# Performance work log

Measured on AMD Instinct MI355X. Metric: run time of the kernel, lower is better.

The kernel has to match this reference:

```python
import jax, jax.numpy as jnp
import numpy as np

S = 32
D = S * S          # d = 1024 grid points
DK = 64
R = 4              # heads
NB = 3             # blocks
IN_DIM = 64
EPS = 1e-5
DX = 2.0 / (S - 1)
DXDY = DX * DX
SCALE = 1.0 / np.sqrt(float(DK))


def _edge():
    # grid[i,j] = (gx[i], gx[j]); gridT is the transpose ordering
    gx = jnp.linspace(-1.0, 1.0, S, dtype=jnp.float32)
    g = jnp.stack(jnp.meshgrid(gx, gx, indexing='ij'), axis=-1)  # [S,S,2]
    grid = g.reshape(D, 2)
    gridT = g.transpose(1, 0, 2).reshape(D, 2)
    return jnp.concatenate([
        jnp.broadcast_to(grid[:, None, :], (D, D, 2)),
        jnp.broadcast_to(gridT[None, :, :], (D, D, 2)),
    ], axis=-1)  # [D, D, 4]


def _mlp(e, W1, b1, W2, b2, W3, b3):
    # DenseNet([4,32,64,1], LeakyReLU): two hidden LeakyReLU layers, linear head
    h = jax.nn.leaky_relu(e @ W1 + b1)
    h = jax.nn.leaky_relu(h @ W2 + b2)
    return h @ W3 + b3


def _ln(v, g, b):
    # LayerNorm over normalized_shape [2d, input_dim] -> reduce last two axes
    m = jnp.mean(v, axis=(1, 2), keepdims=True)
    var = jnp.var(v, axis=(1, 2), keepdims=True)
    return (v - m) * jax.lax.rsqrt(var + EPS) * g + b


def setup_inputs() -> dict:
    key = jax.random.key(0)
    ks = jax.random.split(key, 24)
    f32 = jnp.float32

    def nrm(k, shape, fan):
        return jax.random.normal(k, shape, f32) / np.sqrt(float(fan))

    inp = {
        'x': jax.random.normal(ks[0], (8, D, 1), f32),
        'xy': jax.random.normal(ks[1], (8, 2 * D, IN_DIM), f32),
        'P': jnp.zeros((1,), f32),
        # kernel MLP (edge -> weight)
        'kW1': nrm(ks[2], (4, 32), 4), 'kb1': jnp.zeros((32,), f32),
        'kW2': nrm(ks[3], (32, 64), 32), 'kb2': jnp.zeros((64,), f32),
        'kW3': nrm(ks[4], (64, 1), 64), 'kb3': jnp.zeros((1,), f32),
        # kernelf MLP (edge -> weightf)
        'fW1': nrm(ks[5], (4, 32), 4), 'fb1': jnp.zeros((32,), f32),
        'fW2': nrm(ks[6], (32, 64), 32), 'fb2': jnp.zeros((64,), f32),
        'fW3': nrm(ks[7], (64, 1), 64), 'fb3': jnp.zeros((1,), f32),
        # per-(block, head) Q/K linear layers
        'Wq': nrm(ks[8], (NB, R, IN_DIM, DK), IN_DIM),
        'bq': jnp.zeros((NB, R, DK), f32),
        'Wk': nrm(ks[9], (NB, R, IN_DIM, DK), IN_DIM),
        'bk': jnp.zeros((NB, R, DK), f32),
        # per-block LayerNorm affine params over [2d, input_dim]
        'ln_g': jnp.ones((NB, 2 * D, IN_DIM), f32),
        'ln_b': jnp.zeros((NB, 2 * D, IN_DIM), f32),
    }
    return inp


def _forward(x, xy, P, kW1, kb1, kW2, kb2, kW3, kb3,
             fW1, fb1, fW2, fb2, fW3, fb3, Wq, bq, Wk, bk, ln_g, ln_b):
    edge = _edge()
    weight = _mlp(edge, kW1, kb1, kW2, kb2, kW3, kb3).reshape(D, D)   # shared over batch
    weightf = _mlp(edge, fW1, fb1, fW2, fb2, fW3, fb3).reshape(D, D)

    Vinput = _ln(xy, ln_g[0], ln_b[0])  # [b, 2d, in]

    for j in range(NB - 1):
        mid = jnp.zeros_like(Vinput)
        for i in range(R):
            Q = Vinput @ Wq[j, i] + bq[j, i]  # [b, 2d, dk]
            K = Vinput @ Wk[j, i] + bk[j, i]
            Attn = jnp.einsum('bnk,bmk->bnm', Q, K) * SCALE  # [b, 2d, 2d]
            mid = mid + DXDY * jnp.einsum('bnm,bmi->bni', Attn, Vinput)
        Vinput = _ln(mid, ln_g[j + 1], ln_b[j + 1]) + Vinput

    b = xy.shape[0]
    out = jnp.zeros((b, IN_DIM, D), xy.dtype)
    xy_d = xy[:, :D, :]  # [b, d, in]
    for i in range(R):
        Q = Vinput @ Wq[NB - 1, i] + bq[NB - 1, i]
        K = Vinput @ Wk[NB - 1, i] + bk[NB - 1, i]
        Au = jnp.einsum('bnk,bmk->bnm', Q[:, :D], K[:, :D]) * SCALE  # Attn[:, :d, :d]
        Af = jnp.einsum('bnk,bmk->bnm', Q[:, D:], K[:, :D]) * SCALE  # Attn[:, d:, :d]
        Vu = DXDY * jnp.einsum('bnm,bmi->bin', Au, xy_d)  # [b, in, d]
        Vf = DXDY * jnp.einsum('bnm,bmi->bin', Af, xy_d)
        out = out + DXDY * (Vu @ weight) + DXDY * (Vf @ weightf)
    return out.transpose(0, 2, 1)  # [b, d, in]


def reference(x, xy, P, kW1, kb1, kW2, kb2, kW3, kb3,
              fW1, fb1, fW2, fb2, fW3, fb3, Wq, bq, Wk, bk, ln_g, ln_b):
    return _forward(x, xy, P, kW1, kb1, kW2, kb2, kW3, kb3,
                    fW1, fb1, fW2, fb2, fW3, fb3, Wq, bq, Wk, bk, ln_g, ln_b)
```

## Files before the change

kernel.cpp:

```cpp
#include <hip/hip_runtime.h>

namespace {
constexpr int SD = 1024;
constexpr int TD = 2048;
constexpr int BATCH = 8;
constexpr int RH = 4;
constexpr float EPSc = 1e-5f;
constexpr float DXf = 2.0f / 31.0f;
constexpr float DXDYf = DXf * DXf;
constexpr float SCALEf = 0.125f;
constexpr float CFINAL = DXDYf * DXDYf * SCALEf;

constexpr size_t OFF_V   = 0;
constexpr size_t OFF_MID = OFF_V   + (size_t)BATCH * TD * 64;
constexpr size_t OFF_W   = OFF_MID + (size_t)BATCH * TD * 64;
constexpr size_t OFF_WF  = OFF_W   + (size_t)SD * SD;
constexpr size_t OFF_U1K = OFF_WF  + (size_t)SD * SD;
constexpr size_t OFF_U2K = OFF_U1K + SD * 32;
constexpr size_t OFF_U1F = OFF_U2K + SD * 32;
constexpr size_t OFF_U2F = OFF_U1F + SD * 32;
constexpr size_t OFF_GP  = OFF_U2F + SD * 32;
constexpr size_t OFF_SP  = OFF_GP  + (size_t)BATCH * 32 * 4096;
constexpr size_t OFF_A   = OFF_SP  + BATCH * 32 * 64;
constexpr size_t OFF_RV  = OFF_A   + BATCH * 4096;
constexpr size_t OFF_LNP = OFF_RV  + BATCH * 64;
constexpr size_t OFF_ZU  = OFF_LNP + BATCH * 32 * 2;
constexpr size_t OFF_ZF  = OFF_ZU  + (size_t)SD * 512;
constexpr size_t OFF_W1  = OFF_ZF  + (size_t)SD * 512;
constexpr size_t OFF_CS  = OFF_W1  + SD;
constexpr size_t WS_FLOATS = OFF_CS + 16 * SD;
constexpr size_t LIN_OFF = 50704;
}

typedef __bf16 bf16x8 __attribute__((ext_vector_type(8)));
typedef float f32x4 __attribute__((ext_vector_type(4)));

__device__ __forceinline__ float leaky(float x) { return fmaxf(x, 0.01f * x); }
__device__ __forceinline__ float gxv(int i) { return -1.0f + (2.0f / 31.0f) * (float)i; }
__device__ __forceinline__ ushort f2bf(float x) { union { __bf16 b; ushort u; } v; v.b = (__bf16)x; return v.u; }
__device__ __forceinline__ float bf2f(ushort u) { return __uint_as_float(((uint)u) << 16); }

__global__ __launch_bounds__(256) void k_prep(
    const float* __restrict__ kW1, const float* __restrict__ kb1,
    const float* __restrict__ fW1, const float* __restrict__ fb1,
    float* __restrict__ u1k, float* __restrict__ u2k,
    float* __restrict__ u1f, float* __restrict__ u2f,
    const float* __restrict__ kW2, const float* __restrict__ kW3, const float* __restrict__ kb2,
    const float* __restrict__ fW2, const float* __restrict__ fW3, const float* __restrict__ fb2,
    float* __restrict__ LIN,
    const float* __restrict__ Wq, const float* __restrict__ bq,
    const float* __restrict__ Wk, const float* __restrict__ bk,
    float* __restrict__ Ep, float* __restrict__ fp,
    float* __restrict__ gp, float* __restrict__ cp,
    const float* __restrict__ xy, float* __restrict__ part) {
  __shared__ __align__(16) float Wqs[4096];
  __shared__ float Wks[64 * 65];
  __shared__ float bqs[64], bks[64];
  __shared__ float ss4[4], qq4[4];
  int blk = blockIdx.x, t = threadIdx.x;
  if (blk >= 16) {
    int idx = blk - 16;
    int b = idx >> 5, c = idx & 31;
    const float4* X4 = reinterpret_cast<const float4*>(xy + (size_t)b * 131072 + (size_t)c * 4096);
    float s = 0.f, q = 0.f;
#pragma unroll
    for (int k = 0; k < 4; k++) {
      float4 v = X4[t + k * 256];
      s += v.x + v.y + v.z + v.w;
      q += v.x * v.x + v.y * v.y + v.z * v.z + v.w * v.w;
    }
    for (int off = 32; off; off >>= 1) { s += __shfl_down(s, off); q += __shfl_down(q, off); }
    int lane = t & 63, wid = t >> 6;
    if (lane == 0) { ss4[wid] = s; qq4[wid] = q; }
    __syncthreads();
    if (t == 0) {
      part[(size_t)(b * 32 + c) * 2] = ss4[0] + ss4[1] + ss4[2] + ss4[3];
      part[(size_t)(b * 32 + c) * 2 + 1] = qq4[0] + qq4[1] + qq4[2] + qq4[3];
    }
    return;
  }
  if (blk < 4) {
    int n = blk * 256 + t;
    float ga = gxv(n >> 5), gb = gxv(n & 31);
    for (int j = 0; j < 32; j++) {
      u1k[n * 32 + j] = ga * kW1[j] + gb * kW1[32 + j] + kb1[j];
      u2k[n * 32 + j] = gb * kW1[64 + j] + ga * kW1[96 + j];
      u1f[n * 32 + j] = ga * fW1[j] + gb * fW1[32 + j] + fb1[j];
      u2f[n * 32 + j] = gb * fW1[64 + j] + ga * fW1[96 + j];
    }
    if (blk < 2 && t < 33) {
      const float* W2 = blk ? fW2 : kW2;
      const float* W3 = blk ? fW3 : kW3;
      const float* b2 = blk ? fb2 : kb2;
      if (t < 32) {
        float s = 0.f;
        for (int o = 0; o < 64; o++) s += W2[t * 64 + o] * W3[o];
        LIN[blk * 32 + t] = s;
      } else {
        float s = 0.f;
        for (int o = 0; o < 64; o++) s += b2[o] * W3[o];
        LIN[64 + blk] = s;
      }
    }
    return;
  }
  int h = blk - 4;
  const float* wqb = Wq + (size_t)h * 4096;
  const float* wkb = Wk + (size_t)h * 4096;
  for (int idx = t; idx < 4096; idx += 256) {
    Wqs[idx] = wqb[idx];
    Wks[(idx >> 6) * 65 + (idx & 63)] = wkb[idx];
  }
  if (t < 64) { bqs[t] = bq[h * 64 + t]; bks[t] = bk[h * 64 + t]; }
  __syncthreads();
  int cpp = t & 63, cb = (t >> 6) * 16;
  float acc[16];
#pragma unroll
  for (int u = 0; u < 16; u++) acc[u] = 0.f;
  for (int k = 0; k < 64; k++) {
    float wkv = Wks[cpp * 65 + k];
#pragma unroll
    for (int u = 0; u < 16; u++) acc[u] += Wqs[(cb + u) * 64 + k] * wkv;
  }
  float* eo = Ep + (size_t)h * 4096;
#pragma unroll
  for (int u = 0; u < 16; u++) eo[(cb + u) * 64 + cpp] = acc[u];
  if (t < 64) {
    float f = 0.f, gg = 0.f;
    for (int k = 0; k < 64; k++) {
      f  += Wqs[t * 64 + k] * bks[k];
      gg += Wks[t * 65 + k] * bqs[k];
    }
    fp[h * 64 + t] = f;
    gp[h * 64 + t] = gg;
    float ca = bqs[t] * bks[t];
    ca += __shfl_xor(ca, 1, 64);
    ca += __shfl_xor(ca, 2, 64);
    ca += __shfl_xor(ca, 4, 64);
    ca += __shfl_xor(ca, 8, 64);
    ca += __shfl_xor(ca, 16, 64);
    ca += __shfl_xor(ca, 32, 64);
    if (t == 0) cp[h] = ca;
  }
}

__global__ __launch_bounds__(256) void k_mlp2(
    const float* __restrict__ u1k, const float* __restrict__ u2k,
    const float* __restrict__ kW2, const float* __restrict__ kb2,
    const float* __restrict__ kW3, const float* __restrict__ kb3,
    const float* __restrict__ u1f, const float* __restrict__ u2f,
    const float* __restrict__ fW2, const float* __restrict__ fb2,
    const float* __restrict__ fW3, const float* __restrict__ fb3,
    const float* __restrict__ LIN,
    ushort* __restrict__ outK, ushort* __restrict__ outF) {
  const int which = blockIdx.y;
  const float* u1 = which ? u1f : u1k;
  const float* u2 = which ? u2f : u2k;
  const float* W2 = which ? fW2 : kW2;
  const float* b2 = which ? fb2 : kb2;
  const float* W3 = which ? fW3 : kW3;
  const float* b3 = which ? fb3 : kb3;
  ushort* out = which ? outF : outK;

  const int t = threadIdx.x;
  const int lane = t & 63, wave = t >> 6;
  const int row = lane & 15, grp = lane >> 4;
  const int n0 = (blockIdx.x >> 1) * 2;
  const int mh = blockIdx.x & 1;

  bf16x8 wfrag[4];
  float4 b2q[4], w3q[4];
#pragma unroll
  for (int tt = 0; tt < 4; tt++) {
#pragma unroll
    for (int i = 0; i < 8; i++) wfrag[tt][i] = (__bf16)W2[(grp * 8 + i) * 64 + tt * 16 + row];
    b2q[tt] = *reinterpret_cast<const float4*>(b2 + tt * 16 + grp * 4);
    w3q[tt] = *reinterpret_cast<const float4*>(W3 + tt * 16 + grp * 4);
  }
  float4 l0 = *reinterpret_cast<const float4*>(LIN + which * 32 + grp * 8);
  float4 l1 = *reinterpret_cast<const float4*>(LIN + which * 32 + grp * 8 + 4);
  float linp[8] = {l0.x, l0.y, l0.z, l0.w, l1.x, l1.y, l1.z, l1.w};
  const float cst = 0.505f * LIN[64 + which] + b3[0];

  float u1j[2][8];
#pragma unroll
  for (int nn = 0; nn < 2; nn++)
#pragma unroll
    for (int i = 0; i < 8; i++) u1j[nn][i] = u1[(n0 + nn) * 32 + grp * 8 + i];

#pragma unroll
  for (int chunk = 0; chunk < 2; chunk++) {
#pragma unroll
    for (int st = 0; st < 4; st++) {
      int mbase = mh * 512 + chunk * 256 + wave * 64 + st * 16;
      int m = mbase + row;
      const float4* u2p = reinterpret_cast<const float4*>(u2 + (size_t)m * 32 + grp * 8);
      float4 ua = u2p[0], ub = u2p[1];
      float hv[8] = {ua.x, ua.y, ua.z, ua.w, ub.x, ub.y, ub.z, ub.w};
#pragma unroll
      for (int nn = 0; nn < 2; nn++) {
        float h1f[8];
#pragma unroll
        for (int i = 0; i < 8; i++) h1f[i] = leaky(u1j[nn][i] + hv[i]);
        float accLin = 0.f;
#pragma unroll
        for (int i = 0; i < 8; i++) accLin = fmaf(linp[i], h1f[i], accLin);
        bf16x8 pfrag;
#pragma unroll
        for (int i = 0; i < 8; i++) pfrag[i] = (__bf16)h1f[i];
        float accAbs = 0.f;
#pragma unroll
        for (int tt = 0; tt < 4; tt++) {
          f32x4 ci = {b2q[tt].x, b2q[tt].y, b2q[tt].z, b2q[tt].w};
          f32x4 c = __builtin_amdgcn_mfma_f32_16x16x32_bf16(wfrag[tt], pfrag, ci, 0, 0, 0);
          accAbs = fmaf(fabsf(c[0]), w3q[tt].x, accAbs);
          accAbs = fmaf(fabsf(c[1]), w3q[tt].y, accAbs);
          accAbs = fmaf(fabsf(c[2]), w3q[tt].z, accAbs);
          accAbs = fmaf(fabsf(c[3]), w3q[tt].w, accAbs);
        }
        float red = fmaf(0.495f, accAbs, 0.505f * accLin);
        red += __shfl_xor(red, 16, 64);
        red += __shfl_xor(red, 32, 64);
        if (grp == 0) out[(size_t)(n0 + nn) * SD + mbase + row] = f2bf(red + cst);
      }
    }
  }
}

__global__ __launch_bounds__(256) void k_cvtapply(
    const ushort* __restrict__ srcA, const ushort* __restrict__ srcB,
    ushort* __restrict__ dstA, ushort* __restrict__ dstB,
    const float* __restrict__ src, const float* __restrict__ g,
    const float* __restrict__ bb, const float* __restrict__ lnp,
    float* __restrict__ Vout, float* __restrict__ Gp, float* __restrict__ sp) {
  __shared__ float T[64][65];
  __shared__ __align__(16) float Vs[4096];
  __shared__ float sm[2];
  int blk = blockIdx.x, t = threadIdx.x;
  if (blk < 512) {
    int bx = blk & 15, by = (blk >> 4) & 15, bz = blk >> 8;
    const ushort* srcp = bz ? srcB : srcA;
    ushort* dst = bz ? dstB : dstA;
    int c0 = bx * 64, r0 = by * 64;
    int rr = t >> 2, cc = (t & 3) * 16;
    const uint4* s4 = reinterpret_cast<const uint4*>(srcp + (size_t)(r0 + rr) * 1024 + c0 + cc);
    uint4 q0 = s4[0], q1 = s4[1];
    uint qs[8] = {q0.x, q0.y, q0.z, q0.w, q1.x, q1.y, q1.z, q1.w};
#pragma unroll
    for (int j = 0; j < 8; j++) {
      T[rr][cc + 2 * j]     = bf2f((ushort)(qs[j] & 0xffffu));
      T[rr][cc + 2 * j + 1] = bf2f((ushort)(qs[j] >> 16));
    }
    __syncthreads();
    uint pk[8];
#pragma unroll
    for (int j = 0; j < 8; j++) {
      uint lo = (uint)f2bf(T[cc + 2 * j][rr]);
      uint hi = (uint)f2bf(T[cc + 2 * j + 1][rr]);
      pk[j] = lo | (hi << 16);
    }
    ushort* dp = dst + (size_t)(c0 + rr) * 1024 + r0 + cc;
    uint4* dp4 = reinterpret_cast<uint4*>(dp);
    dp4[0] = make_uint4(pk[0], pk[1], pk[2], pk[3]);
    dp4[1] = make_uint4(pk[4], pk[5], pk[6], pk[7]);
    return;
  }
  int idx2 = blk - 512;
  int c = idx2 & 31, b = idx2 >> 5;
  if (t == 0) {
    float s = 0.f, q = 0.f;
    for (int cc = 0; cc < 32; cc++) {
      s += lnp[(size_t)(b * 32 + cc) * 2];
      q += lnp[(size_t)(b * 32 + cc) * 2 + 1];
    }
    float mean = s / 131072.0f;
    sm[0] = mean;
    sm[1] = rsqrtf(q / 131072.0f - mean * mean + EPSc);
  }
  __syncthreads();
  float mean = sm[0], is = sm[1];
  size_t base4 = (size_t)b * 32768 + (size_t)c * 1024;
#pragma unroll
  for (int k = 0; k < 4; k++) {
    int idx = t + k * 256;
    float4 v = reinterpret_cast<const float4*>(src)[base4 + idx];
    float4 gg = reinterpret_cast<const float4*>(g)[c * 1024 + idx];
    float4 bv = reinterpret_cast<const float4*>(bb)[c * 1024 + idx];
    float4 r;
    r.x = (v.x - mean) * is * gg.x + bv.x;
    r.y = (v.y - mean) * is * gg.y + bv.y;
    r.z = (v.z - mean) * is * gg.z + bv.z;
    r.w = (v.w - mean) * is * gg.w + bv.w;
    reinterpret_cast<float4*>(Vout)[base4 + idx] = r;
    reinterpret_cast<float4*>(Vs)[idx] = r;
  }
  __syncthreads();
  int tp = t >> 4, tq = t & 15;
  float a2[4][4] = {};
  for (int k = 0; k < 64; k++) {
    float4 xv = *reinterpret_cast<const float4*>(&Vs[k * 64 + tp * 4]);
    float4 yv = *reinterpret_cast<const float4*>(&Vs[k * 64 + tq * 4]);
    a2[0][0] += xv.x * yv.x; a2[0][1] += xv.x * yv.y; a2[0][2] += xv.x * yv.z; a2[0][3] += xv.x * yv.w;
    a2[1][0] += xv.y * yv.x; a2[1][1] += xv.y * yv.y; a2[1][2] += xv.y * yv.z; a2[1][3] += xv.y * yv.w;
    a2[2][0] += xv.z * yv.x; a2[2][1] += xv.z * yv.y; a2[2][2] += xv.z * yv.z; a2[2][3] += xv.z * yv.w;
    a2[3][0] += xv.w * yv.x; a2[3][1] += xv.w * yv.y; a2[3][2] += xv.w * yv.z; a2[3][3] += xv.w * yv.w;
  }
  float* go = Gp + (size_t)(b * 32 + c) * 4096;
#pragma unroll
  for (int i = 0; i < 4; i++) {
    float4 w = {a2[i][0], a2[i][1], a2[i][2], a2[i][3]};
    *reinterpret_cast<float4*>(&go[(tp * 4 + i) * 64 + tq * 4]) = w;
  }
  if (t < 64) {
    float s = 0.f;
    for (int k = 0; k < 64; k++) s += Vs[k * 64 + t];
    sp[(size_t)(b * 32 + c) * 64 + t] = s;
  }
}

__global__ __launch_bounds__(256) void k_gred(const float* __restrict__ Gp, const float* __restrict__ sp,
                                              float* __restrict__ G, float* __restrict__ sv, int nch) {
  int blk = blockIdx.x, b = blockIdx.y, t = threadIdx.x;
  int idx = blk * 256 + t;
  float a = 0.f;
  for (int c = 0; c < nch; c++) a += Gp[(size_t)(b * nch + c) * 4096 + idx];
  G[(size_t)b * 4096 + idx] = a;
  if (blk == 0 && t < 64) {
    float s = 0.f;
    for (int c = 0; c < nch; c++) s += sp[(size_t)(b * nch + c) * 64 + t];
    sv[b * 64 + t] = s;
  }
}

__global__ __launch_bounds__(256) void k_headsA2(
    const float* __restrict__ G, const float* __restrict__ sv,
    const float* __restrict__ Ep, const float* __restrict__ fp,
    const float* __restrict__ gp, const float* __restrict__ cp,
    int j, float scale, int doStats,
    float* __restrict__ A, float* __restrict__ RVo, float* __restrict__ STAT) {
  int b = blockIdx.x, t = threadIdx.x;
  __shared__ float Es[64 * 65];
  __shared__ __align__(16) float Gs[4096];
  __shared__ __align__(16) float As[4096];
  __shared__ float ss[64], fs[64], gs[64];
  __shared__ float cj;
  __shared__ float redbuf[8];
  const float* e0 = Ep + (size_t)(j * RH) * 4096;
  for (int idx = t; idx < 4096; idx += 256) {
    float e = e0[idx] + e0[idx + 4096] + e0[idx + 8192] + e0[idx + 12288];
    Es[(idx >> 6) * 65 + (idx & 63)] = e;
    Gs[idx] = G[(size_t)b * 4096 + idx];
  }
  if (t < 64) {
    ss[t] = sv[b * 64 + t];
    int h0 = j * RH * 64;
    fs[t] = fp[h0 + t] + fp[h0 + 64 + t] + fp[h0 + 128 + t] + fp[h0 + 192 + t];
    gs[t] = gp[h0 + t] + gp[h0 + 64 + t] + gp[h0 + 128 + t] + gp[h0 + 192 + t];
  }
  if (t == 0) cj = cp[j * RH] + cp[j * RH + 1] + cp[j * RH + 2] + cp[j * RH + 3];
  __syncthreads();
  int c = t >> 2, qb = (t & 3) * 16;
  float fv = fs[c];
  float4 acc[4];
#pragma unroll
  for (int u = 0; u < 4; u++) {
    acc[u].x = fv * ss[qb + u * 4 + 0];
    acc[u].y = fv * ss[qb + u * 4 + 1];
    acc[u].z = fv * ss[qb + u * 4 + 2];
    acc[u].w = fv * ss[qb + u * 4 + 3];
  }
  for (int d = 0; d < 64; d++) {
    float ev = Es[c * 65 + d];
    const float4* gr = reinterpret_cast<const float4*>(&Gs[d * 64 + qb]);
#pragma unroll
    for (int u = 0; u < 4; u++) {
      float4 gv = gr[u];
      acc[u].x += ev * gv.x; acc[u].y += ev * gv.y; acc[u].z += ev * gv.z; acc[u].w += ev * gv.w;
    }
  }
  float* ao = A + (size_t)b * 4096 + c * 64 + qb;
#pragma unroll
  for (int u = 0; u < 4; u++) {
    float4 v = acc[u];
    v.x *= scale; v.y *= scale; v.z *= scale; v.w *= scale;
    reinterpret_cast<float4*>(ao)[u] = v;
    *reinterpret_cast<float4*>(&As[c * 64 + qb + u * 4]) = v;
  }
  float rv_t = 0.f;
  if (t < 64) {
    float r = cj * ss[t];
    for (int d = 0; d < 64; d++) r += gs[d] * Gs[d * 64 + t];
    r *= scale;
    RVo[b * 64 + t] = r;
    rv_t = r;
  }
  if (!doStats) return;
  __syncthreads();
  float4 h[4] = {};
  for (int d = 0; d < 64; d++) {
    float gvv = Gs[c * 64 + d];
    const float4* ar = reinterpret_cast<const float4*>(&As[d * 64 + qb]);
#pragma unroll
    for (int u = 0; u < 4; u++) {
      float4 av = ar[u];
      h[u].x += gvv * av.x; h[u].y += gvv * av.y; h[u].z += gvv * av.z; h[u].w += gvv * av.w;
    }
  }
  float tp_ = 0.f;
#pragma unroll
  for (int u = 0; u < 4; u++) {
    float4 a = *reinterpret_cast<const float4*>(&As[c * 64 + qb + u * 4]);
    tp_ += a.x * h[u].x + a.y * h[u].y + a.z * h[u].z + a.w * h[u].w;
  }
  tp_ += __shfl_xor(tp_, 1, 64);  tp_ += __shfl_xor(tp_, 2, 64);
  tp_ += __shfl_xor(tp_, 4, 64);  tp_ += __shfl_xor(tp_, 8, 64);
  tp_ += __shfl_xor(tp_, 16, 64); tp_ += __shfl_xor(tp_, 32, 64);
  if ((t & 63) == 0) redbuf[t >> 6] = tp_;
  if (t < 64) {
    float t1 = 0.f;
    for (int d = 0; d < 64; d++) t1 += ss[d] * As[d * 64 + t];
    float s1 = t1, sr = rv_t, sr2 = rv_t * rv_t, srt = rv_t * t1;
#pragma unroll
    for (int off = 1; off < 64; off <<= 1) {
      s1  += __shfl_xor(s1, off, 64);
      sr  += __shfl_xor(sr, off, 64);
      sr2 += __shfl_xor(sr2, off, 64);
      srt += __shfl_xor(srt, off, 64);
    }
    if (t == 0) { redbuf[4] = s1; redbuf[5] = sr; redbuf[6] = sr2; redbuf[7] = srt; }
  }
  __syncthreads();
  if (t == 0) {
    float tr = redbuf[0] + redbuf[1] + redbuf[2] + redbuf[3];
    float smid = redbuf[4] + 2048.0f * redbuf[5];
    float mu = smid / 131072.0f;
    float e2 = (tr + 2.0f * redbuf[7] + 2048.0f * redbuf[6]) / 131072.0f;
    STAT[b * 2] = mu;
    STAT[b * 2 + 1] = rsqrtf(e2 - mu * mu + EPSc);
  }
}

__global__ __launch_bounds__(256) void k_midapply(
    float* __restrict__ V, const float* __restrict__ A,
    const float* __restrict__ RVv, const float* __restrict__ STAT,
    const float* __restrict__ g, const float* __restrict__ bb,
    const float* __restrict__ Yext,
    float* __restrict__ Gp, float* __restrict__ sp, int nchG) {
  int blk = blockIdx.x, b = blockIdx.y, t = threadIdx.x;
  __shared__ __align__(16) float As[4096];
  __shared__ __align__(16) float Vs[4096];
  __shared__ __align__(16) float Ys[4096];
  __shared__ float rs[64];
  __shared__ float sm[2];
  const float4* A4 = reinterpret_cast<const float4*>(A + (size_t)b * 4096);
#pragma unroll
  for (int k = 0; k < 4; k++) reinterpret_cast<float4*>(As)[t + k * 256] = A4[t + k * 256];
  if (t < 64) rs[t] = RVv[b * 64 + t];
  if (t == 0) { sm[0] = STAT[b * 2]; sm[1] = STAT[b * 2 + 1]; }
  bool doG = (blk < nchG);
  if (Yext != nullptr && doG) {
    size_t yb = (size_t)b * 32768 + (size_t)blk * 1024;
#pragma unroll
    for (int k = 0; k < 4; k++)
      reinterpret_cast<float4*>(Ys)[t + k * 256] = reinterpret_cast<const float4*>(Yext)[yb + t + k * 256];
  }
  __syncthreads();
  float mu = sm[0], is = sm[1];
  int rl = t >> 2, qb = (t & 3) * 16;
  int row = blk * 64 + rl;
  float* vr = V + (size_t)b * 131072 + (size_t)row * 64;
  float4 acc[4];
#pragma unroll
  for (int u = 0; u < 4; u++) {
    acc[u].x = rs[qb + u * 4 + 0]; acc[u].y = rs[qb + u * 4 + 1];
    acc[u].z = rs[qb + u * 4 + 2]; acc[u].w = rs[qb + u * 4 + 3];
  }
  for (int c = 0; c < 64; c++) {
    float vv = vr[c];
    const float4* ar = reinterpret_cast<const float4*>(&As[c * 64 + qb]);
#pragma unroll
    for (int u = 0; u < 4; u++) {
      float4 av = ar[u];
      acc[u].x += vv * av.x; acc[u].y += vv * av.y; acc[u].z += vv * av.z; acc[u].w += vv * av.w;
    }
  }
  const float4* g4 = reinterpret_cast<const float4*>(g + (size_t)row * 64 + qb);
  const float4* b4 = reinterpret_cast<const float4*>(bb + (size_t)row * 64 + qb);
  const float4* vq = reinterpret_cast<const float4*>(vr + qb);
  float4* vo = reinterpret_cast<float4*>(vr + qb);
#pragma unroll
  for (int u = 0; u < 4; u++) {
    float4 gg = g4[u], bv = b4[u], av = vq[u];
    float4 r;
    r.x = (acc[u].x - mu) * is * gg.x + bv.x + av.x;
    r.y = (acc[u].y - mu) * is * gg.y + bv.y + av.y;
    r.z = (acc[u].z - mu) * is * gg.z + bv.z + av.z;
    r.w = (acc[u].w - mu) * is * gg.w + bv.w + av.w;
    vo[u] = r;
    *reinterpret_cast<float4*>(&Vs[rl * 64 + qb + u * 4]) = r;
  }
  __syncthreads();
  if (!doG) return;
  const float* Yp = (Yext != nullptr) ? Ys : Vs;
  int tp = t >> 4, tq = t & 15;
  float a2[4][4] = {};
  for (int k = 0; k < 64; k++) {
    float4 xv = *reinterpret_cast<const float4*>(&Vs[k * 64 + tp * 4]);
    float4 yv = *reinterpret_cast<const float4*>(&Yp[k * 64 + tq * 4]);
    a2[0][0] += xv.x * yv.x; a2[0][1] += xv.x * yv.y; a2[0][2] += xv.x * yv.z; a2[0][3] += xv.x * yv.w;
    a2[1][0] += xv.y * yv.x; a2[1][1] += xv.y * yv.y; a2[1][2] += xv.y * yv.z; a2[1][3] += xv.y * yv.w;
    a2[2][0] += xv.z * yv.x; a2[2][1] += xv.z * yv.y; a2[2][2] += xv.z * yv.z; a2[2][3] += xv.z * yv.w;
    a2[3][0] += xv.w * yv.x; a2[3][1] += xv.w * yv.y; a2[3][2] += xv.w * yv.z; a2[3][3] += xv.w * yv.w;
  }
  float* go = Gp + (size_t)(b * nchG + blk) * 4096;
#pragma unroll
  for (int i = 0; i < 4; i++) {
    float4 w = {a2[i][0], a2[i][1], a2[i][2], a2[i][3]};
    *reinterpret_cast<float4*>(&go[(tp * 4 + i) * 64 + tq * 4]) = w;
  }
  if (t < 64) {
    float s = 0.f;
    for (int k = 0; k < 64; k++) s += Yp[k * 64 + t];
    sp[(size_t)(b * nchG + blk) * 64 + t] = s;
  }
}

__global__ __launch_bounds__(256) void k_y(const float* __restrict__ V, const float* __restrict__ A,
                                           ushort* __restrict__ ZT) {
  int blk = blockIdx.x, b = blockIdx.y, z = blockIdx.z, t = threadIdx.x;
  __shared__ __align__(16) float As[4096];
  __shared__ ushort Zs[64][36];
  const float4* A4 = reinterpret_cast<const float4*>(A + (size_t)b * 4096);
#pragma unroll
  for (int k = 0; k < 4; k++) reinterpret_cast<float4*>(As)[t + k * 256] = A4[t + k * 256];
  __syncthreads();
  int ml = t >> 3, qb = (t & 7) * 8;
  int m = blk * 32 + ml;
  const float* vr = V + (size_t)b * 131072 + (size_t)(z * 1024 + m) * 64;
  float4 acc[2] = {};
  for (int c = 0; c < 64; c++) {
    float vv = vr[c];
    const float4* ar = reinterpret_cast<const float4*>(&As[c * 64 + qb]);
#pragma unroll
    for (int u = 0; u < 2; u++) {
      float4 av = ar[u];
      acc[u].x += vv * av.x; acc[u].y += vv * av.y; acc[u].z += vv * av.z; acc[u].w += vv * av.w;
    }
  }
  Zs[qb + 0][ml] = f2bf(acc[0].x); Zs[qb + 1][ml] = f2bf(acc[0].y);
  Zs[qb + 2][ml] = f2bf(acc[0].z); Zs[qb + 3][ml] = f2bf(acc[0].w);
  Zs[qb + 4][ml] = f2bf(acc[1].x); Zs[qb + 5][ml] = f2bf(acc[1].y);
  Zs[qb + 6][ml] = f2bf(acc[1].z); Zs[qb + 7][ml] = f2bf(acc[1].w);
  __syncthreads();
  int rowq = t >> 2, seg = t & 3;
  const ushort* srcp = &Zs[rowq][seg * 8];
  uint p0 = (uint)srcp[0] | ((uint)srcp[1] << 16);
  uint p1 = (uint)srcp[2] | ((uint)srcp[3] << 16);
  uint p2 = (uint)srcp[4] | ((uint)srcp[5] << 16);
  uint p3 = (uint)srcp[6] | ((uint)srcp[7] << 16);
  ushort* dp = ZT + (size_t)(b * 64 + rowq) * 2048 + (size_t)z * 1024 + blk * 32 + seg * 8;
  *reinterpret_cast<uint4*>(dp) = make_uint4(p0, p1, p2, p3);
}

__global__ __launch_bounds__(256) void k_final_mfma2(const ushort* __restrict__ WTW,
                                                     const ushort* __restrict__ WTF,
                                                     const ushort* __restrict__ ZT,
                                                     const float* __restrict__ RV,
                                                     float* __restrict__ out) {
  int tn = blockIdx.x, tb = blockIdx.y, t = threadIdx.x;
  int lane = t & 63, w = t >> 6;
  int wn = w & 1, wb = w >> 1;
  int r = lane & 15, g = lane >> 4;
  int nrow = tn * 32 + wn * 16 + r;
  int bi0 = tb * 64 + wb * 32 + r;
  bf16x8 ones;
#pragma unroll
  for (int i = 0; i < 8; i++) ones[i] = (__bf16)1.0f;
  f32x4 a0 = {0.f, 0.f, 0.f, 0.f}, a1 = a0, aw = a0;
  for (int kz = 0; kz < 4; kz++) {
    const ushort* wbase = (kz < 2) ? WTW : WTF;
    const ushort* wp = wbase + (size_t)nrow * 1024 + (kz & 1) * 512 + g * 8;
    const ushort* zp0 = ZT + (size_t)bi0 * 2048 + kz * 512 + g * 8;
    const ushort* zp1 = zp0 + 16 * 2048;
#pragma unroll 4
    for (int ks = 0; ks < 512; ks += 32) {
      bf16x8 fa  = *reinterpret_cast<const bf16x8*>(wp + ks);
      bf16x8 fb0 = *reinterpret_cast<const bf16x8*>(zp0 + ks);
      bf16x8 fb1 = *reinterpret_cast<const bf16x8*>(zp1 + ks);
      a0 = __builtin_amdgcn_mfma_f32_16x16x32_bf16(fa, fb0, a0, 0, 0, 0);
      a1 = __builtin_amdgcn_mfma_f32_16x16x32_bf16(fa, fb1, a1, 0, 0, 0);
      aw = __builtin_amdgcn_mfma_f32_16x16x32_bf16(fa, ones, aw, 0, 0, 0);
    }
  }
  int nbase = tn * 32 + wn * 16 + g * 4;
  int i0 = wb * 32 + r;
  float rv0 = RV[tb * 64 + i0];
  float rv1 = RV[tb * 64 + i0 + 16];
  float* op = out + (size_t)tb * 65536;
#pragma unroll
  for (int rr = 0; rr < 4; rr++) {
    float w1v = aw[rr];
    op[(size_t)(nbase + rr) * 64 + i0]      = CFINAL * (a0[rr] + w1v * rv0);
    op[(size_t)(nbase + rr) * 64 + i0 + 16] = CFINAL * (a1[rr] + w1v * rv1);
  }
}

extern "C" void kernel_launch(void* const* d_in, const int* in_sizes, int n_in,
                              void* d_out, int out_size, void* d_ws, size_t ws_size,
                              hipStream_t stream) {
  (void)in_sizes; (void)n_in; (void)out_size;
  const float* xy  = (const float*)d_in[1];
  const float* kW1 = (const float*)d_in[3];
  const float* kb1 = (const float*)d_in[4];
  const float* kW2 = (const float*)d_in[5];
  const float* kb2 = (const float*)d_in[6];
  const float* kW3 = (const float*)d_in[7];
  const float* kb3 = (const float*)d_in[8];
  const float* fW1 = (const float*)d_in[9];
  const float* fb1 = (const float*)d_in[10];
  const float* fW2 = (const float*)d_in[11];
  const float* fb2 = (const float*)d_in[12];
  const float* fW3 = (const float*)d_in[13];
  const float* fb3 = (const float*)d_in[14];
  const float* Wq  = (const float*)d_in[15];
  const float* bq  = (const float*)d_in[16];
  const float* Wk  = (const float*)d_in[17];
  const float* bk  = (const float*)d_in[18];
  const float* lng = (const float*)d_in[19];
  const float* lnb = (const float*)d_in[20];
  float* ws = (float*)d_ws;
  float* out = (float*)d_out;
  if (ws_size < WS_FLOATS * sizeof(float)) return;

  float* V   = ws + OFF_V;
  float* U1K = ws + OFF_U1K;
  float* U2K = ws + OFF_U2K;
  float* U1F = ws + OFF_U1F;
  float* U2F = ws + OFF_U2F;
  float* GPb = ws + OFF_GP;
  float* SPb = ws + OFF_SP;
  float* LNP = ws + OFF_LNP;
  float* G    = ws + OFF_U1K;
  float* SV   = ws + OFF_U1F;
  float* A    = ws + OFF_A;
  float* RV   = ws + OFF_RV;
  float* STAT = ws + OFF_LNP;
  ushort* Wbf  = (ushort*)(ws + OFF_W);
  ushort* WTW  = (ushort*)(ws + OFF_W + 524288);
  ushort* Wfbf = (ushort*)(ws + OFF_WF);
  ushort* WTF  = (ushort*)(ws + OFF_WF + 524288);
  ushort* ZT   = (ushort*)(ws + OFF_MID);
  float* Ep   = ws + OFF_ZU;
  float* Fp   = ws + OFF_ZU + 49152;
  float* Gpp  = ws + OFF_ZU + 49920;
  float* Cp   = ws + OFF_ZU + 50688;
  float* LIN  = ws + OFF_ZU + LIN_OFF;

  k_prep<<<dim3(272), dim3(256), 0, stream>>>(kW1, kb1, fW1, fb1, U1K, U2K, U1F, U2F,
                                              kW2, kW3, kb2, fW2, fW3, fb2, LIN,
                                              Wq, bq, Wk, bk, Ep, Fp, Gpp, Cp,
                                              xy, LNP);
  k_mlp2<<<dim3(1024, 2), dim3(256), 0, stream>>>(U1K, U2K, kW2, kb2, kW3, kb3,
                                                  U1F, U2F, fW2, fb2, fW3, fb3, LIN, Wbf, Wfbf);
  k_cvtapply<<<dim3(768), dim3(256), 0, stream>>>(Wbf, Wfbf, WTW, WTF,
                                                  xy, lng, lnb, LNP, V, GPb, SPb);

  for (int j = 0; j < 2; j++) {
    k_gred<<<dim3(16, 8), dim3(256), 0, stream>>>(GPb, SPb, G, SV, 32);
    k_headsA2<<<dim3(8), dim3(256), 0, stream>>>(G, SV, Ep, Fp, Gpp, Cp, j, DXDYf * SCALEf, 1,
                                                 A, RV, STAT);
    k_midapply<<<dim3(32, 8), dim3(256), 0, stream>>>(
        V, A, RV, STAT, lng + (size_t)(j + 1) * 131072, lnb + (size_t)(j + 1) * 131072,
        (j == 1) ? xy : nullptr, GPb, SPb, (j == 1) ? 16 : 32);
  }
  k_gred<<<dim3(16, 8), dim3(256), 0, stream>>>(GPb, SPb, G, SV, 16);
  k_headsA2<<<dim3(8), dim3(256), 0, stream>>>(G, SV, Ep, Fp, Gpp, Cp, 2, 1.0f, 0, A, RV, STAT);
  k_y<<<dim3(32, 8, 2), dim3(256), 0, stream>>>(V, A, ZT);
  k_final_mfma2<<<dim3(32, 8), dim3(256), 0, stream>>>(WTW, WTF, ZT, RV, out);
}
```

Before: 181.4 us.

## Regroup kernels: fuse MLP with LN-apply, fuse transpose with first G reduction

The edge-MLP kernel now runs in the same launch as the LayerNorm-apply/Gram-partial blocks, and each MLP block handles 4 rows instead of 2, giving 1024 MLP blocks. The bf16 transpose of the kernel weights moves into a new launch that also does the first Gram reduction, so one k_gred launch disappears. The loop is rotated so the remaining reductions follow each midapply. This cuts launch count and lets independent work share launches, at the cost of more registers per MLP block and mixed block types in one grid.

```diff
diff --git a/kernel.cpp b/kernel.cpp
--- a/kernel.cpp
+++ b/kernel.cpp
@@ -144,7 +144,7 @@
   }
 }
 
-__global__ __launch_bounds__(256) void k_mlp2(
+__global__ __launch_bounds__(256) void k_mlp2apply(
     const float* __restrict__ u1k, const float* __restrict__ u2k,
     const float* __restrict__ kW2, const float* __restrict__ kb2,
     const float* __restrict__ kW3, const float* __restrict__ kb3,
@@ -152,120 +152,89 @@
     const float* __restrict__ fW2, const float* __restrict__ fb2,
     const float* __restrict__ fW3, const float* __restrict__ fb3,
     const float* __restrict__ LIN,
-    ushort* __restrict__ outK, ushort* __restrict__ outF) {
-  const int which = blockIdx.y;
-  const float* u1 = which ? u1f : u1k;
-  const float* u2 = which ? u2f : u2k;
-  const float* W2 = which ? fW2 : kW2;
-  const float* b2 = which ? fb2 : kb2;
-  const float* W3 = which ? fW3 : kW3;
-  const float* b3 = which ? fb3 : kb3;
-  ushort* out = which ? outF : outK;
-
-  const int t = threadIdx.x;
-  const int lane = t & 63, wave = t >> 6;
-  const int row = lane & 15, grp = lane >> 4;
-  const int n0 = (blockIdx.x >> 1) * 2;
-  const int mh = blockIdx.x & 1;
-
-  bf16x8 wfrag[4];
-  float4 b2q[4], w3q[4];
-#pragma unroll
-  for (int tt = 0; tt < 4; tt++) {
-#pragma unroll
-    for (int i = 0; i < 8; i++) wfrag[tt][i] = (__bf16)W2[(grp * 8 + i) * 64 + tt * 16 + row];
-    b2q[tt] = *reinterpret_cast<const float4*>(b2 + tt * 16 + grp * 4);
-    w3q[tt] = *reinterpret_cast<const float4*>(W3 + tt * 16 + grp * 4);
-  }
-  float4 l0 = *reinterpret_cast<const float4*>(LIN + which * 32 + grp * 8);
-  float4 l1 = *reinterpret_cast<const float4*>(LIN + which * 32 + grp * 8 + 4);
-  float linp[8] = {l0.x, l0.y, l0.z, l0.w, l1.x, l1.y, l1.z, l1.w};
-  const float cst = 0.505f * LIN[64 + which] + b3[0];
-
-  float u1j[2][8];
-#pragma unroll
-  for (int nn = 0; nn < 2; nn++)
-#pragma unroll
-    for (int i = 0; i < 8; i++) u1j[nn][i] = u1[(n0 + nn) * 32 + grp * 8 + i];
-
-#pragma unroll
-  for (int chunk = 0; chunk < 2; chunk++) {
-#pragma unroll
-    for (int st = 0; st < 4; st++) {
-      int mbase = mh * 512 + chunk * 256 + wave * 64 + st * 16;
-      int m = mbase + row;
-      const float4* u2p = reinterpret_cast<const float4*>(u2 + (size_t)m * 32 + grp * 8);
-      float4 ua = u2p[0], ub = u2p[1];
-      float hv[8] = {ua.x, ua.y, ua.z, ua.w, ub.x, ub.y, ub.z, ub.w};
-#pragma unroll
-      for (int nn = 0; nn < 2; nn++) {
-        float h1f[8];
-#pragma unroll
-        for (int i = 0; i < 8; i++) h1f[i] = leaky(u1j[nn][i] + hv[i]);
-        float accLin = 0.f;
-#pragma unroll
-        for (int i = 0; i < 8; i++) accLin = fmaf(linp[i], h1f[i], accLin);
-        bf16x8 pfrag;
-#pragma unroll
-        for (int i = 0; i < 8; i++) pfrag[i] = (__bf16)h1f[i];
-        float accAbs = 0.f;
-#pragma unroll
-        for (int tt = 0; tt < 4; tt++) {
-          f32x4 ci = {b2q[tt].x, b2q[tt].y, b2q[tt].z, b2q[tt].w};
-          f32x4 c = __builtin_amdgcn_mfma_f32_16x16x32_bf16(wfrag[tt], pfrag, ci, 0, 0, 0);
-          accAbs = fmaf(fabsf(c[0]), w3q[tt].x, accAbs);
-          accAbs = fmaf(fabsf(c[1]), w3q[tt].y, accAbs);
-          accAbs = fmaf(fabsf(c[2]), w3q[tt].z, accAbs);
-          accAbs = fmaf(fabsf(c[3]), w3q[tt].w, accAbs);
-        }
-        float red = fmaf(0.495f, accAbs, 0.505f * accLin);
-        red += __shfl_xor(red, 16, 64);
-        red += __shfl_xor(red, 32, 64);
-        if (grp == 0) out[(size_t)(n0 + nn) * SD + mbase + row] = f2bf(red + cst);
-      }
-    }
-  }
-}
-
-__global__ __launch_bounds__(256) void k_cvtapply(
-    const ushort* __restrict__ srcA, const ushort* __restrict__ srcB,
-    ushort* __restrict__ dstA, ushort* __restrict__ dstB,
+    ushort* __restrict__ outK, ushort* __restrict__ outF,
     const float* __restrict__ src, const float* __restrict__ g,
     const float* __restrict__ bb, const float* __restrict__ lnp,
     float* __restrict__ Vout, float* __restrict__ Gp, float* __restrict__ sp) {
-  __shared__ float T[64][65];
   __shared__ __align__(16) float Vs[4096];
   __shared__ float sm[2];
-  int blk = blockIdx.x, t = threadIdx.x;
-  if (blk < 512) {
-    int bx = blk & 15, by = (blk >> 4) & 15, bz = blk >> 8;
-    const ushort* srcp = bz ? srcB : srcA;
-    ushort* dst = bz ? dstB : dstA;
-    int c0 = bx * 64, r0 = by * 64;
-    int rr = t >> 2, cc = (t & 3) * 16;
-    const uint4* s4 = reinterpret_cast<const uint4*>(srcp + (size_t)(r0 + rr) * 1024 + c0 + cc);
-    uint4 q0 = s4[0], q1 = s4[1];
-    uint qs[8] = {q0.x, q0.y, q0.z, q0.w, q1.x, q1.y, q1.z, q1.w};
-#pragma unroll
-    for (int j = 0; j < 8; j++) {
-      T[rr][cc + 2 * j]     = bf2f((ushort)(qs[j] & 0xffffu));
-      T[rr][cc + 2 * j + 1] = bf2f((ushort)(qs[j] >> 16));
-    }
-    __syncthreads();
-    uint pk[8];
-#pragma unroll
-    for (int j = 0; j < 8; j++) {
-      uint lo = (uint)f2bf(T[cc + 2 * j][rr]);
-      uint hi = (uint)f2bf(T[cc + 2 * j + 1][rr]);
-      pk[j] = lo | (hi << 16);
-    }
-    ushort* dp = dst + (size_t)(c0 + rr) * 1024 + r0 + cc;
-    uint4* dp4 = reinterpret_cast<uint4*>(dp);
-    dp4[0] = make_uint4(pk[0], pk[1], pk[2], pk[3]);
-    dp4[1] = make_uint4(pk[4], pk[5], pk[6], pk[7]);
+  int blk = blockIdx.x;
+  const int t = threadIdx.x;
+  if (blk < 1024) {
+    const int which = blk >> 9;
+    const int nb = blk & 511;
+    const float* u1 = which ? u1f : u1k;
+    const float* u2 = which ? u2f : u2k;
+    const float* W2 = which ? fW2 : kW2;
+    const float* b2 = which ? fb2 : kb2;
+    const float* W3 = which ? fW3 : kW3;
+    const float* b3 = which ? fb3 : kb3;
+    ushort* out = which ? outF : outK;
+    const int lane = t & 63, wave = t >> 6;
+    const int row = lane & 15, grp = lane >> 4;
+    const int n0 = (nb >> 1) * 4;
+    const int mh = nb & 1;
+
+    bf16x8 wfrag[4];
+    float4 b2q[4], w3q[4];
+#pragma unroll
+    for (int tt = 0; tt < 4; tt++) {
+#pragma unroll
+      for (int i = 0; i < 8; i++) wfrag[tt][i] = (__bf16)W2[(grp * 8 + i) * 64 + tt * 16 + row];
+      b2q[tt] = *reinterpret_cast<const float4*>(b2 + tt * 16 + grp * 4);
+      w3q[tt] = *reinterpret_cast<const float4*>(W3 + tt * 16 + grp * 4);
+    }
+    float4 l0 = *reinterpret_cast<const float4*>(LIN + which * 32 + grp * 8);
+    float4 l1 = *reinterpret_cast<const float4*>(LIN + which * 32 + grp * 8 + 4);
+    float linp[8] = {l0.x, l0.y, l0.z, l0.w, l1.x, l1.y, l1.z, l1.w};
+    const float cst = 0.505f * LIN[64 + which] + b3[0];
+
+    float u1j[4][8];
+#pragma unroll
+    for (int nn = 0; nn < 4; nn++)
+#pragma unroll
+      for (int i = 0; i < 8; i++) u1j[nn][i] = u1[(n0 + nn) * 32 + grp * 8 + i];
+
+#pragma unroll
+    for (int chunk = 0; chunk < 2; chunk++) {
+#pragma unroll
+      for (int st = 0; st < 4; st++) {
+        int mbase = mh * 512 + chunk * 256 + wave * 64 + st * 16;
+        int m = mbase + row;
+        const float4* u2p = reinterpret_cast<const float4*>(u2 + (size_t)m * 32 + grp * 8);
+        float4 ua = u2p[0], ub = u2p[1];
+        float hv[8] = {ua.x, ua.y, ua.z, ua.w, ub.x, ub.y, ub.z, ub.w};
+#pragma unroll
+        for (int nn = 0; nn < 4; nn++) {
+          float h1f[8];
+#pragma unroll
+          for (int i = 0; i < 8; i++) h1f[i] = leaky(u1j[nn][i] + hv[i]);
+          float accLin = 0.f;
+#pragma unroll
+          for (int i = 0; i < 8; i++) accLin = fmaf(linp[i], h1f[i], accLin);
+          bf16x8 pfrag;
+#pragma unroll
+          for (int i = 0; i < 8; i++) pfrag[i] = (__bf16)h1f[i];
+          float accAbs = 0.f;
+#pragma unroll
+          for (int tt = 0; tt < 4; tt++) {
+            f32x4 ci = {b2q[tt].x, b2q[tt].y, b2q[tt].z, b2q[tt].w};
+            f32x4 c = __builtin_amdgcn_mfma_f32_16x16x32_bf16(wfrag[tt], pfrag, ci, 0, 0, 0);
+            accAbs = fmaf(fabsf(c[0]), w3q[tt].x, accAbs);
+            accAbs = fmaf(fabsf(c[1]), w3q[tt].y, accAbs);
+            accAbs = fmaf(fabsf(c[2]), w3q[tt].z, accAbs);
+            accAbs = fmaf(fabsf(c[3]), w3q[tt].w, accAbs);
+          }
+          float red = fmaf(0.495f, accAbs, 0.505f * accLin);
+          red += __shfl_xor(red, 16, 64);
+          red += __shfl_xor(red, 32, 64);
+          if (grp == 0) out[(size_t)(n0 + nn) * SD + mbase + row] = f2bf(red + cst);
+        }
+      }
+    }
     return;
   }
-  int idx2 = blk - 512;
+  int idx2 = blk - 1024;
   int c = idx2 & 31, b = idx2 >> 5;
   if (t == 0) {
     float s = 0.f, q = 0.f;
@@ -315,6 +284,54 @@
     float s = 0.f;
     for (int k = 0; k < 64; k++) s += Vs[k * 64 + t];
     sp[(size_t)(b * 32 + c) * 64 + t] = s;
+  }
+}
+
+__global__ __launch_bounds__(256) void k_cvtgred(
+    const ushort* __restrict__ srcA, const ushort* __restrict__ srcB,
+    ushort* __restrict__ dstA, ushort* __restrict__ dstB,
+    const float* __restrict__ Gp, const float* __restrict__ sp,
+    float* __restrict__ G, float* __restrict__ sv) {
+  __shared__ float T[64][65];
+  int blk = blockIdx.x, t = threadIdx.x;
+  if (blk < 512) {
+    int bx = blk & 15, by = (blk >> 4) & 15, bz = blk >> 8;
+    const ushort* srcp = bz ? srcB : srcA;
+    ushort* dst = bz ? dstB : dstA;
+    int c0 = bx * 64, r0 = by * 64;
+    int rr = t >> 2, cc = (t & 3) * 16;
+    const uint4* s4 = reinterpret_cast<const uint4*>(srcp + (size_t)(r0 + rr) * 1024 + c0 + cc);
+    uint4 q0 = s4[0], q1 = s4[1];
+    uint qs[8] = {q0.x, q0.y, q0.z, q0.w, q1.x, q1.y, q1.z, q1.w};
+#pragma unroll
+    for (int j = 0; j < 8; j++) {
+      T[rr][cc + 2 * j]     = bf2f((ushort)(qs[j] & 0xffffu));
+      T[rr][cc + 2 * j + 1] = bf2f((ushort)(qs[j] >> 16));
+    }
+    __syncthreads();
+    uint pk[8];
+#pragma unroll
+    for (int j = 0; j < 8; j++) {
+      uint lo = (uint)f2bf(T[cc + 2 * j][rr]);
+      uint hi = (uint)f2bf(T[cc + 2 * j + 1][rr]);
+      pk[j] = lo | (hi << 16);
+    }
+    ushort* dp = dst + (size_t)(c0 + rr) * 1024 + r0 + cc;
+    uint4* dp4 = reinterpret_cast<uint4*>(dp);
+    dp4[0] = make_uint4(pk[0], pk[1], pk[2], pk[3]);
+    dp4[1] = make_uint4(pk[4], pk[5], pk[6], pk[7]);
+    return;
+  }
+  int idx2 = blk - 512;
+  int gblk = idx2 & 15, b = idx2 >> 4;
+  int idx = gblk * 256 + t;
+  float a = 0.f;
+  for (int c = 0; c < 32; c++) a += Gp[(size_t)(b * 32 + c) * 4096 + idx];
+  G[(size_t)b * 4096 + idx] = a;
+  if (gblk == 0 && t < 64) {
+    float s = 0.f;
+    for (int c = 0; c < 32; c++) s += sp[(size_t)(b * 32 + c) * 64 + t];
+    sv[b * 64 + t] = s;
   }
 }
 
@@ -660,20 +677,19 @@
                                               kW2, kW3, kb2, fW2, fW3, fb2, LIN,
                                               Wq, bq, Wk, bk, Ep, Fp, Gpp, Cp,
                                               xy, LNP);
-  k_mlp2<<<dim3(1024, 2), dim3(256), 0, stream>>>(U1K, U2K, kW2, kb2, kW3, kb3,
-                                                  U1F, U2F, fW2, fb2, fW3, fb3, LIN, Wbf, Wfbf);
-  k_cvtapply<<<dim3(768), dim3(256), 0, stream>>>(Wbf, Wfbf, WTW, WTF,
-                                                  xy, lng, lnb, LNP, V, GPb, SPb);
+  k_mlp2apply<<<dim3(1280), dim3(256), 0, stream>>>(U1K, U2K, kW2, kb2, kW3, kb3,
+                                                    U1F, U2F, fW2, fb2, fW3, fb3, LIN, Wbf, Wfbf,
+                                                    xy, lng, lnb, LNP, V, GPb, SPb);
+  k_cvtgred<<<dim3(640), dim3(256), 0, stream>>>(Wbf, Wfbf, WTW, WTF, GPb, SPb, G, SV);
 
   for (int j = 0; j < 2; j++) {
-    k_gred<<<dim3(16, 8), dim3(256), 0, stream>>>(GPb, SPb, G, SV, 32);
     k_headsA2<<<dim3(8), dim3(256), 0, stream>>>(G, SV, Ep, Fp, Gpp, Cp, j, DXDYf * SCALEf, 1,
                                                  A, RV, STAT);
     k_midapply<<<dim3(32, 8), dim3(256), 0, stream>>>(
         V, A, RV, STAT, lng + (size_t)(j + 1) * 131072, lnb + (size_t)(j + 1) * 131072,
         (j == 1) ? xy : nullptr, GPb, SPb, (j == 1) ? 16 : 32);
-  }
-  k_gred<<<dim3(16, 8), dim3(256), 0, stream>>>(GPb, SPb, G, SV, 16);
+    k_gred<<<dim3(16, 8), dim3(256), 0, stream>>>(GPb, SPb, G, SV, (j == 1) ? 16 : 32);
+  }
   k_headsA2<<<dim3(8), dim3(256), 0, stream>>>(G, SV, Ep, Fp, Gpp, Cp, 2, 1.0f, 0, A, RV, STAT);
   k_y<<<dim3(32, 8, 2), dim3(256), 0, stream>>>(V, A, ZT);
   k_final_mfma2<<<dim3(32, 8), dim3(256), 0, stream>>>(WTW, WTF, ZT, RV, out);
```

After: 160.3 us. 1.13x faster.
